# Kernel optimization log

Measured on AMD Instinct MI355X. Metric: run time of the kernel, lower is better.

## Reference

```python
import jax, jax.numpy as jnp
import numpy as np

N = 50000        # nodes
E = 500000       # undirected edges (stored once)
D = 64           # n_in_features
DOUT = 64        # n_out_features
HLF = 2          # hl_factor
NCONV = 3        # n_conv_its
H = D * HLF      # hidden width of conv MLPs


def setup_inputs() -> dict:
    key = jax.random.key(0)
    ks = jax.random.split(key, 8)
    s = 0.05
    edge_features = jax.random.normal(ks[0], (E, D), jnp.float32)
    edge_index = jax.random.randint(ks[1], (2, E), 0, N, dtype=jnp.int64)
    node_w1 = jax.random.normal(ks[2], (NCONV, 2 * D, H), jnp.float32) * s
    node_b1 = jnp.zeros((NCONV, H), jnp.float32)
    node_w2 = jax.random.normal(ks[3], (NCONV, H, D), jnp.float32) * s
    node_b2 = jnp.zeros((NCONV, D), jnp.float32)
    edge_w1 = jax.random.normal(ks[4], (2 * D, H), jnp.float32) * s
    edge_b1 = jnp.zeros((H,), jnp.float32)
    edge_w2 = jax.random.normal(ks[5], (H, DOUT), jnp.float32) * s
    edge_b2 = jnp.zeros((DOUT,), jnp.float32)
    return dict(edge_features=edge_features, edge_index=edge_index,
                node_w1=node_w1, node_b1=node_b1, node_w2=node_w2, node_b2=node_b2,
                edge_w1=edge_w1, edge_b1=edge_b1, edge_w2=edge_w2, edge_b2=edge_b2)


def _seg_mean(x, idx, n):
    s = jax.ops.segment_sum(x, idx, num_segments=n)
    c = jax.ops.segment_sum(jnp.ones((idx.shape[0], 1), x.dtype), idx, num_segments=n)
    return s / jnp.maximum(c, 1.0)


def reference(edge_features, edge_index, node_w1, node_b1, node_w2, node_b2,
              edge_w1, edge_b1, edge_w2, edge_b2):
    src, dst = edge_index[0], edge_index[1]
    # bidirectional (symmetrized) edges for message passing
    bi_src = jnp.concatenate([src, dst])
    bi_dst = jnp.concatenate([dst, src])

    # EdgeConvNoNodes: node feature = mean of incident edge features
    x = _seg_mean(jnp.concatenate([edge_features, edge_features], axis=0), bi_dst, N)  # [N, D]

    # NodeConv layers with residual: message = MLP(cat[x_i, x_j]), mean-aggregated
    for i in range(NCONV):
        m = jnp.concatenate([x[bi_dst], x[bi_src]], axis=-1)        # [2E, 2D]
        m = jax.nn.relu(m @ node_w1[i] + node_b1[i])                # [2E, H]
        m = jax.nn.relu(m @ node_w2[i] + node_b2[i])                # [2E, D]
        x = x + _seg_mean(m, bi_dst, N)

    # EdgeConv: symmetric edge MLP over node endpoint pairs + symmetry side loss
    def emlp(a, b):
        h = jax.nn.relu(jnp.concatenate([a, b], axis=-1) @ edge_w1 + edge_b1)
        return h @ edge_w2 + edge_b2

    e1 = emlp(x[src], x[dst])   # [E, DOUT]
    e2 = emlp(x[dst], x[src])   # [E, DOUT]
    edge_out = 0.5 * (e1 + e2)
    side_loss = jnp.mean((e1 - e2) ** 2)
    return edge_out, side_loss
```

## Files before the change

### kernel.cpp

```cpp
#include <hip/hip_runtime.h>


#define NN 50000
#define NE 500000
#define DE 1000000
#define NEB 7813

typedef __attribute__((ext_vector_type(8))) __bf16 bfrag;
typedef __attribute__((ext_vector_type(8))) short  svec8;
typedef __attribute__((ext_vector_type(4))) float  f32x4;

__device__ __forceinline__ unsigned short f2bf(float f){
  unsigned u = __builtin_bit_cast(unsigned, f);
  u += 0x7fffu + ((u >> 16) & 1u);
  return (unsigned short)(u >> 16);
}
__device__ __forceinline__ float bf2f(unsigned short s){
  return __builtin_bit_cast(float, ((unsigned)s) << 16);
}
#define MFMA __builtin_amdgcn_mfma_f32_16x16x32_bf16

__device__ __forceinline__ bfrag hbuild2(svec8 pv, svec8 qv){
  bfrag r;
  #pragma unroll
  for (int i = 0; i < 8; i++){
    float f = bf2f((unsigned short)pv[i]) + bf2f((unsigned short)qv[i]);
    f = f > 0.f ? f : 0.f;
    r[i] = (__bf16)f;
  }
  return r;
}

__global__ void k_hist(const int* __restrict__ ei, int* __restrict__ cnt,
                       int* __restrict__ cnt2){
  int e = blockIdx.x*256 + threadIdx.x;
  if (e >= DE) return;
  int dst = (e < NE) ? ei[NE + e] : ei[e - NE];
  atomicAdd(&cnt[dst], 1);
  if (e < NE) atomicAdd(&cnt2[ei[e]], 1);
}

__device__ __forceinline__ void scan_impl(const int* __restrict__ cnt,
                                          int* __restrict__ off, int* __restrict__ cur,
                                          float* __restrict__ dinv, int total){
  __shared__ int wsum[16];
  __shared__ int carry_s;
  int tid = threadIdx.x;
  int lane = tid & 63, w = tid >> 6;
  int carry = 0;
  for (int base = 0; base < NN; base += 1024){
    int idx = base + tid;
    int v = (idx < NN) ? cnt[idx] : 0;
    int inc = v;
    for (int o2 = 1; o2 < 64; o2 <<= 1){
      int t = __shfl_up(inc, o2);
      if (lane >= o2) inc += t;
    }
    if (lane == 63) wsum[w] = inc;
    __syncthreads();
    if (tid < 16){
      int vv = wsum[tid], p = vv;
      for (int o2 = 1; o2 < 16; o2 <<= 1){
        int t = __shfl_up(p, o2, 16);
        if (tid >= o2) p += t;
      }
      wsum[tid] = p - vv;
    }
    __syncthreads();
    int ex = carry + wsum[w] + inc - v;
    if (idx < NN){
      off[idx] = ex; cur[idx] = ex;
      dinv[idx] = 1.0f / (float)(v > 1 ? v : 1);
    }
    if (tid == 1023) carry_s = carry + wsum[15] + inc;
    __syncthreads();
    carry = carry_s;
  }
  if (tid == 0) off[NN] = total;
}

__global__ void k_scan2(const int* __restrict__ cntA, int* __restrict__ offA,
                        int* __restrict__ curA, float* __restrict__ dinvA,
                        const int* __restrict__ cntB, int* __restrict__ offB,
                        int* __restrict__ curB, float* __restrict__ dinvB){
  if (blockIdx.x == 0) scan_impl(cntA, offA, curA, dinvA, DE);
  else                 scan_impl(cntB, offB, curB, dinvB, NE);
}

__global__ void k_fill(const int* __restrict__ ei, int* __restrict__ cur,
                       int* __restrict__ nbr, int* __restrict__ dstA, int* __restrict__ eid,
                       int* __restrict__ cur2, int* __restrict__ eord,
                       int* __restrict__ es, int* __restrict__ ed){
  int e = blockIdx.x*256 + threadIdx.x;
  if (e >= DE) return;
  int s, d, id;
  if (e < NE){ s = ei[e];  d = ei[NE + e]; id = e;      }
  else       { s = ei[e];  d = ei[e - NE]; id = e - NE; }
  int pos = atomicAdd(&cur[d], 1);
  nbr[pos] = s; dstA[pos] = d; eid[pos] = id;
  if (e < NE){
    int p2 = atomicAdd(&cur2[s], 1);
    eord[p2] = e; es[p2] = s; ed[p2] = d;
  }
}

__global__ void k_pack(const float* __restrict__ nw1, const float* __restrict__ nw2,
                       const float* __restrict__ ew1, const float* __restrict__ ew2,
                       unsigned short* __restrict__ wp){
  int t = blockIdx.x*256 + threadIdx.x;
  if (t >= 98304) return;
  const float* src; int NO, p, base;
  if (t < 49152)      { int l = t/16384;            src = nw1 + l*16384; NO=128; p = t - l*16384;      base = t - p; }
  else if (t < 73728) { int q = t-49152; int l=q/8192; src = nw2 + l*8192; NO=64; p = q - l*8192;      base = t - p; }
  else if (t < 90112) {                              src = ew1;           NO=128; p = t - 73728;       base = 73728; }
  else                {                              src = ew2;           NO=64;  p = t - 90112;       base = 90112; }
  int f = p >> 9, r = p & 511, lane = r >> 3, i = r & 7;
  int NB = NO >> 4, kb = f / NB, nb = f - kb*NB;
  int k = kb*32 + ((lane >> 4) << 3) + i;
  int c = nb*16 + (lane & 15);
  wp[base + p] = f2bf(src[k*NO + c]);
}

__global__ __launch_bounds__(256,4) void k_init(
    const float* __restrict__ ef, const int* __restrict__ dstA,
    const int* __restrict__ eid, float* __restrict__ xsum)
{
  int lane = threadIdx.x & 63, wid = threadIdx.x >> 6;
  int tile = (blockIdx.x*4 + wid) * 32;
  if (tile >= DE) return;
  int q = lane >> 4, c4 = lane & 15;
  int dr = dstA[tile + (lane & 31)];
  int er = eid[tile + (lane & 31)];
  f32x4 v[8];
  #pragma unroll
  for (int it = 0; it < 8; it++){
    int row = q + it*4;
    int e = __shfl(er, row);
    v[it] = *(const f32x4*)(ef + (size_t)e*64 + c4*4);
  }
  int prev = __shfl_up(dr, 1);
  bool flag = (lane < 32) && (lane == 0 || dr != prev);
  unsigned long long mask = __ballot(flag);
  while (mask){
    int s = (int)__builtin_ctzll(mask);
    mask &= mask - 1;
    int e = mask ? (int)__builtin_ctzll(mask) : 32;
    int dseg = __shfl(dr, s);
    f32x4 p = {0,0,0,0};
    #pragma unroll
    for (int it = 0; it < 8; it++){
      int row = q + it*4;
      if ((unsigned)(row - s) < (unsigned)(e - s)) p += v[it];
    }
    #pragma unroll
    for (int k = 0; k < 4; k++){
      p[k] += __shfl_xor(p[k], 16);
      p[k] += __shfl_xor(p[k], 32);
    }
    if (q == 0){
      atomicAdd(&xsum[dseg*64 + c4*4 + 0], p[0]);
      atomicAdd(&xsum[dseg*64 + c4*4 + 1], p[1]);
      atomicAdd(&xsum[dseg*64 + c4*4 + 2], p[2]);
      atomicAdd(&xsum[dseg*64 + c4*4 + 3], p[3]);
    }
  }
}

__global__ void k_div(const float* __restrict__ xsum, const float* __restrict__ dinv,
                      float* __restrict__ x, unsigned short* __restrict__ xbf){
  int n = blockIdx.x*4 + (threadIdx.x >> 6);
  int lane = threadIdx.x & 63;
  if (n >= NN) return;
  float v = xsum[n*64 + lane] * dinv[n];
  x[n*64 + lane] = v;
  xbf[n*64 + lane] = f2bf(v);
}

__global__ __launch_bounds__(256,2) void k_pq(
    const unsigned short* __restrict__ xbf,
    const unsigned short* __restrict__ wp, int w1off,
    const float* __restrict__ bias,
    unsigned short* __restrict__ pq)
{
  int lane = threadIdx.x & 63, wid = threadIdx.x >> 6;
  int tile = (blockIdx.x*4 + wid) * 32;
  if (tile >= NN) return;
  int r16 = lane & 15, g = lane >> 4;
  const svec8* w1g = (const svec8*)(wp + w1off);
  bfrag a[2][2];
  #pragma unroll
  for (int rb = 0; rb < 2; rb++){
    int n = tile + rb*16 + r16; if (n >= NN) n = NN-1;
    #pragma unroll
    for (int kb = 0; kb < 2; kb++)
      a[rb][kb] = __builtin_bit_cast(bfrag, *(const svec8*)(xbf + n*64 + kb*32 + g*8));
  }
  for (int ph = 0; ph < 2; ph++){
    f32x4 acc[8][2];
    #pragma unroll
    for (int nb = 0; nb < 8; nb++){ acc[nb][0] = (f32x4){0,0,0,0}; acc[nb][1] = (f32x4){0,0,0,0}; }
    #pragma unroll
    for (int kb = 0; kb < 2; kb++){
      #pragma unroll
      for (int nb = 0; nb < 8; nb++){
        bfrag b = __builtin_bit_cast(bfrag, w1g[((ph*2+kb)*8+nb)*64 + lane]);
        acc[nb][0] = MFMA(a[0][kb], b, acc[nb][0], 0, 0, 0);
        acc[nb][1] = MFMA(a[1][kb], b, acc[nb][1], 0, 0, 0);
      }
    }
    int half = ph ? 128 : 0;
    #pragma unroll
    for (int nb = 0; nb < 8; nb++){
      float bv = (ph == 0) ? bias[nb*16 + r16] : 0.f;
      #pragma unroll
      for (int rb = 0; rb < 2; rb++){
        #pragma unroll
        for (int j = 0; j < 4; j++){
          int n = tile + rb*16 + g*4 + j;
          if (n < NN) pq[(size_t)n*256 + half + nb*16 + r16] = f2bf(acc[nb][rb][j] + bv);
        }
      }
    }
  }
}

__global__ __launch_bounds__(256,3) void k_conv(
    const unsigned short* __restrict__ pq,
    const int* __restrict__ cdst, const int* __restrict__ cnbr,
    const unsigned short* __restrict__ wp, int w2off,
    const float* __restrict__ b2, float* __restrict__ xsum)
{
  int lane = threadIdx.x & 63, wid = threadIdx.x >> 6;
  int tile = (blockIdx.x*4 + wid) * 32;
  if (tile >= DE) return;
  int r16 = lane & 15, g = lane >> 4;
  int dr = cdst[tile + (lane & 31)];
  int d0 = cdst[tile + r16],      d1 = cdst[tile + 16 + r16];
  int s0 = cnbr[tile + r16],      s1 = cnbr[tile + 16 + r16];
  const svec8* w2g = (const svec8*)(wp + w2off);

  svec8 LP0[4], LQ0[4], LP1[4], LQ1[4];
  #pragma unroll
  for (int kb = 0; kb < 4; kb++){
    int off = kb*32 + g*8;
    LP0[kb] = *(const svec8*)(pq + (size_t)d0*256 + off);
    LQ0[kb] = *(const svec8*)(pq + (size_t)s0*256 + 128 + off);
    LP1[kb] = *(const svec8*)(pq + (size_t)d1*256 + off);
    LQ1[kb] = *(const svec8*)(pq + (size_t)s1*256 + 128 + off);
  }

  f32x4 acc[4][2];
  #pragma unroll
  for (int nb = 0; nb < 4; nb++){ acc[nb][0] = (f32x4){0,0,0,0}; acc[nb][1] = (f32x4){0,0,0,0}; }

  #pragma unroll
  for (int kb = 0; kb < 4; kb++){
    bfrag h0 = hbuild2(LP0[kb], LQ0[kb]);
    bfrag h1 = hbuild2(LP1[kb], LQ1[kb]);
    #pragma unroll
    for (int nb = 0; nb < 4; nb++){
      bfrag b = __builtin_bit_cast(bfrag, w2g[(kb*4+nb)*64 + lane]);
      acc[nb][0] = MFMA(h0, b, acc[nb][0], 0, 0, 0);
      acc[nb][1] = MFMA(h1, b, acc[nb][1], 0, 0, 0);
    }
  }
  float m[4][2][4];
  #pragma unroll
  for (int nb = 0; nb < 4; nb++){
    float bv = b2[nb*16 + r16];
    #pragma unroll
    for (int rb = 0; rb < 2; rb++){
      #pragma unroll
      for (int j = 0; j < 4; j++){
        float v = acc[nb][rb][j] + bv;
        m[nb][rb][j] = v > 0.f ? v : 0.f;
      }
    }
  }
  int prev = __shfl_up(dr, 1);
  bool flag = (lane < 32) && (lane == 0 || dr != prev);
  unsigned long long mask = __ballot(flag);
  while (mask){
    int s = (int)__builtin_ctzll(mask);
    mask &= mask - 1;
    int e = mask ? (int)__builtin_ctzll(mask) : 32;
    int dseg = __shfl(dr, s);
    float p0 = 0.f, p1 = 0.f, p2 = 0.f, p3 = 0.f;
    #pragma unroll
    for (int rb = 0; rb < 2; rb++){
      #pragma unroll
      for (int j = 0; j < 4; j++){
        int row = rb*16 + g*4 + j;
        if ((unsigned)(row - s) < (unsigned)(e - s)){
          p0 += m[0][rb][j]; p1 += m[1][rb][j]; p2 += m[2][rb][j]; p3 += m[3][rb][j];
        }
      }
    }
    p0 += __shfl_xor(p0, 16); p0 += __shfl_xor(p0, 32);
    p1 += __shfl_xor(p1, 16); p1 += __shfl_xor(p1, 32);
    p2 += __shfl_xor(p2, 16); p2 += __shfl_xor(p2, 32);
    p3 += __shfl_xor(p3, 16); p3 += __shfl_xor(p3, 32);
    if (g == 0){
      atomicAdd(&xsum[dseg*64 +      r16], p0);
      atomicAdd(&xsum[dseg*64 + 16 + r16], p1);
      atomicAdd(&xsum[dseg*64 + 32 + r16], p2);
      atomicAdd(&xsum[dseg*64 + 48 + r16], p3);
    }
  }
}

__global__ void k_finish(const float* __restrict__ xsum, const float* __restrict__ dinv,
                         float* __restrict__ x, unsigned short* __restrict__ xbf){
  int n = blockIdx.x*4 + (threadIdx.x >> 6);
  int lane = threadIdx.x & 63;
  if (n >= NN) return;
  float v = x[n*64 + lane] + xsum[n*64 + lane] * dinv[n];
  x[n*64 + lane] = v;
  xbf[n*64 + lane] = f2bf(v);
}

__global__ __launch_bounds__(256,3) void k_edge(
    const unsigned short* __restrict__ pq,
    const int* __restrict__ eord, const int* __restrict__ es, const int* __restrict__ ed,
    const unsigned short* __restrict__ wp,
    const float* __restrict__ b2,
    float* __restrict__ outp, float* __restrict__ part)
{
  __shared__ float wred[4];
  int lane = threadIdx.x & 63, wid = threadIdx.x >> 6;
  int tile = (blockIdx.x*4 + wid) * 16;
  bool valid = tile < NE;
  int tl = valid ? tile : 0;
  int r16 = lane & 15, g = lane >> 4;
  const svec8* w2g = (const svec8*)(wp + 90112);
  int eidv = eord[tl + r16];
  int sid  = es[tl + r16], did = ed[tl + r16];

  svec8 SP[4], SQ[4], DP[4], DQ[4];
  #pragma unroll
  for (int kb = 0; kb < 4; kb++){
    int off = kb*32 + g*8;
    SP[kb] = *(const svec8*)(pq + (size_t)sid*256 + off);
    SQ[kb] = *(const svec8*)(pq + (size_t)sid*256 + 128 + off);
    DP[kb] = *(const svec8*)(pq + (size_t)did*256 + off);
    DQ[kb] = *(const svec8*)(pq + (size_t)did*256 + 128 + off);
  }

  f32x4 acc[4][2];
  #pragma unroll
  for (int nb = 0; nb < 4; nb++){ acc[nb][0] = (f32x4){0,0,0,0}; acc[nb][1] = (f32x4){0,0,0,0}; }

  #pragma unroll
  for (int kb = 0; kb < 4; kb++){
    bfrag h0 = hbuild2(SP[kb], DQ[kb]);
    bfrag h1 = hbuild2(DP[kb], SQ[kb]);
    #pragma unroll
    for (int nb = 0; nb < 4; nb++){
      bfrag b = __builtin_bit_cast(bfrag, w2g[(kb*4+nb)*64 + lane]);
      acc[nb][0] = MFMA(h0, b, acc[nb][0], 0, 0, 0);
      acc[nb][1] = MFMA(h1, b, acc[nb][1], 0, 0, 0);
    }
  }
  float lsum = 0.f;
  #pragma unroll
  for (int nb = 0; nb < 4; nb++){
    float bv = b2[nb*16 + r16];
    #pragma unroll
    for (int j = 0; j < 4; j++){
      float v1 = acc[nb][0][j] + bv;
      float v2 = acc[nb][1][j] + bv;
      int eo = __shfl(eidv, g*4 + j);
      if (valid) outp[(size_t)eo*64 + nb*16 + r16] = 0.5f*(v1 + v2);
      float d = v1 - v2; lsum += d*d;
    }
  }
  if (!valid) lsum = 0.f;
  for (int o2 = 32; o2 > 0; o2 >>= 1) lsum += __shfl_down(lsum, o2);
  if (lane == 0) wred[wid] = lsum;
  __syncthreads();
  if (threadIdx.x == 0) part[blockIdx.x] = wred[0] + wred[1] + wred[2] + wred[3];
}

__global__ void k_final(const float* __restrict__ part, float* __restrict__ outp){
  __shared__ float wred[16];
  int tid = threadIdx.x;
  float s = 0.f;
  for (int i = tid; i < NEB; i += 1024) s += part[i];
  for (int o2 = 32; o2 > 0; o2 >>= 1) s += __shfl_down(s, o2);
  int lane = tid & 63, w = tid >> 6;
  if (lane == 0) wred[w] = s;
  __syncthreads();
  if (tid == 0){
    float t = 0.f;
    #pragma unroll
    for (int i = 0; i < 16; i++) t += wred[i];
    outp[32000000] = t * (1.0f / 32000000.0f);
  }
}

extern "C" void kernel_launch(void* const* d_in, const int* in_sizes, int n_in,
                              void* d_out, int out_size, void* d_ws, size_t ws_size,
                              hipStream_t stream)
{
  const float* ef  = (const float*)d_in[0];
  const int*   ei  = (const int*)  d_in[1];
  const float* nw1 = (const float*)d_in[2];
  const float* nb1 = (const float*)d_in[3];
  const float* nw2 = (const float*)d_in[4];
  const float* nb2 = (const float*)d_in[5];
  const float* ew1 = (const float*)d_in[6];
  const float* eb1 = (const float*)d_in[7];
  const float* ew2 = (const float*)d_in[8];
  const float* eb2 = (const float*)d_in[9];
  float* outp = (float*)d_out;

  char* ws = (char*)d_ws;
  size_t o = 0;
  auto alloc = [&](size_t b)->char*{ char* p = ws + o; o += (b + 255) & ~(size_t)255; return p; };
  int*   cnt  = (int*)  alloc((size_t)NN*4);
  int*   off  = (int*)  alloc((size_t)(NN+1)*4);
  int*   cur  = (int*)  alloc((size_t)NN*4);
  float* dinv = (float*)alloc((size_t)NN*4);
  int*   cnt2 = (int*)  alloc((size_t)NN*4);
  int*   off2 = (int*)  alloc((size_t)(NN+1)*4);
  int*   cur2 = (int*)  alloc((size_t)NN*4);
  float* dinvS= (float*)alloc((size_t)NN*4);
  int*   nbr  = (int*)  alloc((size_t)DE*4);
  int*   dstA = (int*)  alloc((size_t)DE*4);
  int*   eid  = (int*)  alloc((size_t)DE*4);
  int*   eord = (int*)  alloc((size_t)NE*4);
  int*   es   = (int*)  alloc((size_t)NE*4);
  int*   ed   = (int*)  alloc((size_t)NE*4);
  float* x    = (float*)alloc((size_t)NN*64*4);
  unsigned short* xbf = (unsigned short*)alloc((size_t)NN*64*2);
  unsigned short* wp  = (unsigned short*)alloc((size_t)98304*2);
  float* part = (float*)alloc((size_t)NEB*4);
  unsigned short* pq  = (unsigned short*)alloc((size_t)NN*256*2);
  float* xsI  = (float*)alloc((size_t)NN*64*4);
  float* xs0  = (float*)alloc((size_t)NN*64*4);
  float* xs1  = (float*)alloc((size_t)NN*64*4);
  float* xs2  = (float*)alloc((size_t)NN*64*4);
  float* xsum[3] = {xs0, xs1, xs2};

  hipMemsetAsync(cnt,  0, (size_t)NN*4, stream);
  hipMemsetAsync(cnt2, 0, (size_t)NN*4, stream);
  hipMemsetAsync(xsI, 0, (size_t)NN*64*4, stream);
  hipMemsetAsync(xs0, 0, (size_t)NN*64*4, stream);
  hipMemsetAsync(xs1, 0, (size_t)NN*64*4, stream);
  hipMemsetAsync(xs2, 0, (size_t)NN*64*4, stream);
  k_hist<<<(DE+255)/256, 256, 0, stream>>>(ei, cnt, cnt2);
  k_scan2<<<2, 1024, 0, stream>>>(cnt, off, cur, dinv, cnt2, off2, cur2, dinvS);
  k_fill<<<(DE+255)/256, 256, 0, stream>>>(ei, cur, nbr, dstA, eid, cur2, eord, es, ed);
  k_pack<<<384, 256, 0, stream>>>(nw1, nw2, ew1, ew2, wp);
  k_init<<<NEB, 256, 0, stream>>>(ef, dstA, eid, xsI);
  k_div<<<NN/4 + 1, 256, 0, stream>>>(xsI, dinv, x, xbf);
  for (int l = 0; l < 3; l++){
    k_pq<<<391, 256, 0, stream>>>(xbf, wp, l*16384, nb1 + l*128, pq);
    k_conv<<<DE/128 + 1, 256, 0, stream>>>(pq, dstA, nbr, wp,
                                           49152 + l*8192, nb2 + l*64, xsum[l]);
    k_finish<<<NN/4 + 1, 256, 0, stream>>>(xsum[l], dinv, x, xbf);
  }
  k_pq<<<391, 256, 0, stream>>>(xbf, wp, 73728, eb1, pq);
  k_edge<<<NEB, 256, 0, stream>>>(pq, eord, es, ed, wp, eb2, outp, part);
  k_final<<<1, 1024, 0, stream>>>(part, outp);
}
```

Baseline: 723.4 us.

## Fuse node update into projection kernel and software-pipeline persistent conv/edge tiles

Removes the separate k_div and k_finish kernels. k_pq now reads the fp32 aggregate, applies the degree normalisation and residual add, writes x, and converts to bf16 in-register. k_conv and k_edge become persistent-style kernels: each wave handles 8 consecutive tiles and double-buffers its gather loads, so the next tile's pq rows are fetched while the current tile's MFMAs run. Register pressure rises from the doubled buffers, which drops occupancy to 2 waves per SIMD, and the fixed 1024-block grid reduces the partial-sum count.

New measurement: 911.2 us. 26.0% more time.

```diff
diff --git a/kernel.cpp b/kernel.cpp
--- a/kernel.cpp
+++ b/kernel.cpp
@@ -5,6 +5,9 @@
 #define NE 500000
 #define DE 1000000
 #define NEB 7813
+#define NPB 1024
+#define NT  31250
+#define CH  8
 
 typedef __attribute__((ext_vector_type(8))) __bf16 bfrag;
 typedef __attribute__((ext_vector_type(8))) short  svec8;
@@ -166,18 +169,9 @@
   }
 }
 
-__global__ void k_div(const float* __restrict__ xsum, const float* __restrict__ dinv,
-                      float* __restrict__ x, unsigned short* __restrict__ xbf){
-  int n = blockIdx.x*4 + (threadIdx.x >> 6);
-  int lane = threadIdx.x & 63;
-  if (n >= NN) return;
-  float v = xsum[n*64 + lane] * dinv[n];
-  x[n*64 + lane] = v;
-  xbf[n*64 + lane] = f2bf(v);
-}
-
 __global__ __launch_bounds__(256,2) void k_pq(
-    const unsigned short* __restrict__ xbf,
+    float* __restrict__ x, const float* __restrict__ xs, const float* __restrict__ dinv,
+    int mode,
     const unsigned short* __restrict__ wp, int w1off,
     const float* __restrict__ bias,
     unsigned short* __restrict__ pq)
@@ -190,10 +184,28 @@
   bfrag a[2][2];
   #pragma unroll
   for (int rb = 0; rb < 2; rb++){
-    int n = tile + rb*16 + r16; if (n >= NN) n = NN-1;
-    #pragma unroll
-    for (int kb = 0; kb < 2; kb++)
-      a[rb][kb] = __builtin_bit_cast(bfrag, *(const svec8*)(xbf + n*64 + kb*32 + g*8));
+    int n0 = tile + rb*16 + r16;
+    bool vrow = n0 < NN;
+    int n = vrow ? n0 : NN-1;
+    float dv = dinv[n];
+    #pragma unroll
+    for (int kb = 0; kb < 2; kb++){
+      size_t base = (size_t)n*64 + kb*32 + g*8;
+      f32x4 sa = *(const f32x4*)(xs + base);
+      f32x4 sb = *(const f32x4*)(xs + base + 4);
+      f32x4 xa = {0,0,0,0}, xb = {0,0,0,0};
+      if (mode){ xa = *(const f32x4*)(x + base); xb = *(const f32x4*)(x + base + 4); }
+      f32x4 na = xa + sa*dv;
+      f32x4 nb_ = xb + sb*dv;
+      if (vrow){
+        *(f32x4*)(x + base) = na;
+        *(f32x4*)(x + base + 4) = nb_;
+      }
+      bfrag av;
+      #pragma unroll
+      for (int i = 0; i < 4; i++){ av[i] = (__bf16)na[i]; av[4+i] = (__bf16)nb_[i]; }
+      a[rb][kb] = av;
+    }
   }
   for (int ph = 0; ph < 2; ph++){
     f32x4 acc[8][2];
@@ -224,102 +236,155 @@
   }
 }
 
-__global__ __launch_bounds__(256,3) void k_conv(
+#define CLOAD(dr_, sr_, P0_, Q0_, P1_, Q1_, tt) do{                          \
+  dr_ = cdst[(tt)*32 + (lane & 31)];                                         \
+  sr_ = cnbr[(tt)*32 + (lane & 31)];                                         \
+  int d0_ = __shfl(dr_, r16), d1_ = __shfl(dr_, 16 + r16);                   \
+  int s0_ = __shfl(sr_, r16), s1_ = __shfl(sr_, 16 + r16);                   \
+  _Pragma("unroll")                                                          \
+  for (int kb = 0; kb < 4; kb++){                                            \
+    int off = kb*32 + g*8;                                                   \
+    P0_[kb] = *(const svec8*)(pq + (size_t)d0_*256 + off);                   \
+    Q0_[kb] = *(const svec8*)(pq + (size_t)s0_*256 + 128 + off);             \
+    P1_[kb] = *(const svec8*)(pq + (size_t)d1_*256 + off);                   \
+    Q1_[kb] = *(const svec8*)(pq + (size_t)s1_*256 + 128 + off);             \
+  }                                                                          \
+}while(0)
+
+#define CCOMP(dr_, P0_, Q0_, P1_, Q1_) do{                                   \
+  f32x4 acc[4][2];                                                           \
+  _Pragma("unroll")                                                          \
+  for (int nb = 0; nb < 4; nb++){ acc[nb][0] = (f32x4){0,0,0,0}; acc[nb][1] = (f32x4){0,0,0,0}; } \
+  _Pragma("unroll")                                                          \
+  for (int kb = 0; kb < 4; kb++){                                            \
+    bfrag h0 = hbuild2(P0_[kb], Q0_[kb]);                                    \
+    bfrag h1 = hbuild2(P1_[kb], Q1_[kb]);                                    \
+    _Pragma("unroll")                                                        \
+    for (int nb = 0; nb < 4; nb++){                                          \
+      bfrag b = __builtin_bit_cast(bfrag, w2g[(kb*4+nb)*64 + lane]);         \
+      acc[nb][0] = MFMA(h0, b, acc[nb][0], 0, 0, 0);                         \
+      acc[nb][1] = MFMA(h1, b, acc[nb][1], 0, 0, 0);                         \
+    }                                                                        \
+  }                                                                          \
+  float m[4][2][4];                                                          \
+  _Pragma("unroll")                                                          \
+  for (int nb = 0; nb < 4; nb++){                                            \
+    _Pragma("unroll")                                                        \
+    for (int rb = 0; rb < 2; rb++){                                          \
+      _Pragma("unroll")                                                      \
+      for (int j = 0; j < 4; j++){                                           \
+        float v = acc[nb][rb][j] + bv[nb];                                   \
+        m[nb][rb][j] = v > 0.f ? v : 0.f;                                    \
+      }                                                                      \
+    }                                                                        \
+  }                                                                          \
+  int prev = __shfl_up(dr_, 1);                                              \
+  bool flag = (lane < 32) && (lane == 0 || dr_ != prev);                     \
+  unsigned long long mask = __ballot(flag);                                  \
+  while (mask){                                                              \
+    int s = (int)__builtin_ctzll(mask);                                      \
+    mask &= mask - 1;                                                        \
+    int e = mask ? (int)__builtin_ctzll(mask) : 32;                          \
+    int dseg = __shfl(dr_, s);                                               \
+    float p0 = 0.f, p1 = 0.f, p2 = 0.f, p3 = 0.f;                            \
+    _Pragma("unroll")                                                        \
+    for (int rb = 0; rb < 2; rb++){                                          \
+      _Pragma("unroll")                                                      \
+      for (int j = 0; j < 4; j++){                                           \
+        int row = rb*16 + g*4 + j;                                           \
+        if ((unsigned)(row - s) < (unsigned)(e - s)){                        \
+          p0 += m[0][rb][j]; p1 += m[1][rb][j]; p2 += m[2][rb][j]; p3 += m[3][rb][j]; \
+        }                                                                    \
+      }                                                                      \
+    }                                                                        \
+    p0 += __shfl_xor(p0, 16); p0 += __shfl_xor(p0, 32);                      \
+    p1 += __shfl_xor(p1, 16); p1 += __shfl_xor(p1, 32);                      \
+    p2 += __shfl_xor(p2, 16); p2 += __shfl_xor(p2, 32);                      \
+    p3 += __shfl_xor(p3, 16); p3 += __shfl_xor(p3, 32);                      \
+    if (g == 0){                                                             \
+      atomicAdd(&xsum[dseg*64 +      r16], p0);                              \
+      atomicAdd(&xsum[dseg*64 + 16 + r16], p1);                              \
+      atomicAdd(&xsum[dseg*64 + 32 + r16], p2);                              \
+      atomicAdd(&xsum[dseg*64 + 48 + r16], p3);                              \
+    }                                                                        \
+  }                                                                          \
+}while(0)
+
+__global__ __launch_bounds__(256,2) void k_conv(
     const unsigned short* __restrict__ pq,
     const int* __restrict__ cdst, const int* __restrict__ cnbr,
     const unsigned short* __restrict__ wp, int w2off,
     const float* __restrict__ b2, float* __restrict__ xsum)
 {
   int lane = threadIdx.x & 63, wid = threadIdx.x >> 6;
-  int tile = (blockIdx.x*4 + wid) * 32;
-  if (tile >= DE) return;
+  int wgid = blockIdx.x*4 + wid;
   int r16 = lane & 15, g = lane >> 4;
-  int dr = cdst[tile + (lane & 31)];
-  int d0 = cdst[tile + r16],      d1 = cdst[tile + 16 + r16];
-  int s0 = cnbr[tile + r16],      s1 = cnbr[tile + 16 + r16];
   const svec8* w2g = (const svec8*)(wp + w2off);
-
-  svec8 LP0[4], LQ0[4], LP1[4], LQ1[4];
+  int t0 = wgid*CH, t1 = t0 + CH; if (t1 > NT) t1 = NT;
+  if (t0 >= t1) return;
+  float bv[4];
   #pragma unroll
-  for (int kb = 0; kb < 4; kb++){
-    int off = kb*32 + g*8;
-    LP0[kb] = *(const svec8*)(pq + (size_t)d0*256 + off);
-    LQ0[kb] = *(const svec8*)(pq + (size_t)s0*256 + 128 + off);
-    LP1[kb] = *(const svec8*)(pq + (size_t)d1*256 + off);
-    LQ1[kb] = *(const svec8*)(pq + (size_t)s1*256 + 128 + off);
-  }
-
-  f32x4 acc[4][2];
-  #pragma unroll
-  for (int nb = 0; nb < 4; nb++){ acc[nb][0] = (f32x4){0,0,0,0}; acc[nb][1] = (f32x4){0,0,0,0}; }
-
-  #pragma unroll
-  for (int kb = 0; kb < 4; kb++){
-    bfrag h0 = hbuild2(LP0[kb], LQ0[kb]);
-    bfrag h1 = hbuild2(LP1[kb], LQ1[kb]);
-    #pragma unroll
-    for (int nb = 0; nb < 4; nb++){
-      bfrag b = __builtin_bit_cast(bfrag, w2g[(kb*4+nb)*64 + lane]);
-      acc[nb][0] = MFMA(h0, b, acc[nb][0], 0, 0, 0);
-      acc[nb][1] = MFMA(h1, b, acc[nb][1], 0, 0, 0);
-    }
-  }
-  float m[4][2][4];
-  #pragma unroll
-  for (int nb = 0; nb < 4; nb++){
-    float bv = b2[nb*16 + r16];
-    #pragma unroll
-    for (int rb = 0; rb < 2; rb++){
-      #pragma unroll
-      for (int j = 0; j < 4; j++){
-        float v = acc[nb][rb][j] + bv;
-        m[nb][rb][j] = v > 0.f ? v : 0.f;
-      }
-    }
-  }
-  int prev = __shfl_up(dr, 1);
-  bool flag = (lane < 32) && (lane == 0 || dr != prev);
-  unsigned long long mask = __ballot(flag);
-  while (mask){
-    int s = (int)__builtin_ctzll(mask);
-    mask &= mask - 1;
-    int e = mask ? (int)__builtin_ctzll(mask) : 32;
-    int dseg = __shfl(dr, s);
-    float p0 = 0.f, p1 = 0.f, p2 = 0.f, p3 = 0.f;
-    #pragma unroll
-    for (int rb = 0; rb < 2; rb++){
-      #pragma unroll
-      for (int j = 0; j < 4; j++){
-        int row = rb*16 + g*4 + j;
-        if ((unsigned)(row - s) < (unsigned)(e - s)){
-          p0 += m[0][rb][j]; p1 += m[1][rb][j]; p2 += m[2][rb][j]; p3 += m[3][rb][j];
-        }
-      }
-    }
-    p0 += __shfl_xor(p0, 16); p0 += __shfl_xor(p0, 32);
-    p1 += __shfl_xor(p1, 16); p1 += __shfl_xor(p1, 32);
-    p2 += __shfl_xor(p2, 16); p2 += __shfl_xor(p2, 32);
-    p3 += __shfl_xor(p3, 16); p3 += __shfl_xor(p3, 32);
-    if (g == 0){
-      atomicAdd(&xsum[dseg*64 +      r16], p0);
-      atomicAdd(&xsum[dseg*64 + 16 + r16], p1);
-      atomicAdd(&xsum[dseg*64 + 32 + r16], p2);
-      atomicAdd(&xsum[dseg*64 + 48 + r16], p3);
-    }
-  }
-}
-
-__global__ void k_finish(const float* __restrict__ xsum, const float* __restrict__ dinv,
-                         float* __restrict__ x, unsigned short* __restrict__ xbf){
-  int n = blockIdx.x*4 + (threadIdx.x >> 6);
-  int lane = threadIdx.x & 63;
-  if (n >= NN) return;
-  float v = x[n*64 + lane] + xsum[n*64 + lane] * dinv[n];
-  x[n*64 + lane] = v;
-  xbf[n*64 + lane] = f2bf(v);
-}
-
-__global__ __launch_bounds__(256,3) void k_edge(
+  for (int nb = 0; nb < 4; nb++) bv[nb] = b2[nb*16 + r16];
+
+  int drA, srA, drB, srB;
+  svec8 PA0[4], QA0[4], PA1[4], QA1[4];
+  svec8 PB0[4], QB0[4], PB1[4], QB1[4];
+  CLOAD(drA, srA, PA0, QA0, PA1, QA1, t0);
+  for (int t = t0; t < t1; ){
+    int tb = t + 1;
+    if (tb < t1) CLOAD(drB, srB, PB0, QB0, PB1, QB1, tb);
+    CCOMP(drA, PA0, QA0, PA1, QA1);
+    t = tb;
+    if (t >= t1) break;
+    int tc = t + 1;
+    if (tc < t1) CLOAD(drA, srA, PA0, QA0, PA1, QA1, tc);
+    CCOMP(drB, PB0, QB0, PB1, QB1);
+    t = tc;
+  }
+}
+
+#define ELOAD(ev_, SP_, SQ_, DP_, DQ_, tt) do{                               \
+  ev_ = eord[(tt)*16 + r16];                                                 \
+  int sid_ = es[(tt)*16 + r16], did_ = ed[(tt)*16 + r16];                    \
+  _Pragma("unroll")                                                          \
+  for (int kb = 0; kb < 4; kb++){                                            \
+    int off = kb*32 + g*8;                                                   \
+    SP_[kb] = *(const svec8*)(pq + (size_t)sid_*256 + off);                  \
+    SQ_[kb] = *(const svec8*)(pq + (size_t)sid_*256 + 128 + off);            \
+    DP_[kb] = *(const svec8*)(pq + (size_t)did_*256 + off);                  \
+    DQ_[kb] = *(const svec8*)(pq + (size_t)did_*256 + 128 + off);            \
+  }                                                                          \
+}while(0)
+
+#define ECOMP(ev_, SP_, SQ_, DP_, DQ_) do{                                   \
+  f32x4 acc[4][2];                                                           \
+  _Pragma("unroll")                                                          \
+  for (int nb = 0; nb < 4; nb++){ acc[nb][0] = (f32x4){0,0,0,0}; acc[nb][1] = (f32x4){0,0,0,0}; } \
+  _Pragma("unroll")                                                          \
+  for (int kb = 0; kb < 4; kb++){                                            \
+    bfrag h0 = hbuild2(SP_[kb], DQ_[kb]);                                    \
+    bfrag h1 = hbuild2(DP_[kb], SQ_[kb]);                                    \
+    _Pragma("unroll")                                                        \
+    for (int nb = 0; nb < 4; nb++){                                          \
+      bfrag b = __builtin_bit_cast(bfrag, w2g[(kb*4+nb)*64 + lane]);         \
+      acc[nb][0] = MFMA(h0, b, acc[nb][0], 0, 0, 0);                         \
+      acc[nb][1] = MFMA(h1, b, acc[nb][1], 0, 0, 0);                         \
+    }                                                                        \
+  }                                                                          \
+  _Pragma("unroll")                                                          \
+  for (int nb = 0; nb < 4; nb++){                                            \
+    _Pragma("unroll")                                                        \
+    for (int j = 0; j < 4; j++){                                             \
+      float v1 = acc[nb][0][j] + bv[nb];                                     \
+      float v2 = acc[nb][1][j] + bv[nb];                                     \
+      int eo = __shfl(ev_, g*4 + j);                                         \
+      outp[(size_t)eo*64 + nb*16 + r16] = 0.5f*(v1 + v2);                    \
+      float d = v1 - v2; lsum += d*d;                                        \
+    }                                                                        \
+  }                                                                          \
+}while(0)
+
+__global__ __launch_bounds__(256,2) void k_edge(
     const unsigned short* __restrict__ pq,
     const int* __restrict__ eord, const int* __restrict__ es, const int* __restrict__ ed,
     const unsigned short* __restrict__ wp,
@@ -328,53 +393,31 @@
 {
   __shared__ float wred[4];
   int lane = threadIdx.x & 63, wid = threadIdx.x >> 6;
-  int tile = (blockIdx.x*4 + wid) * 16;
-  bool valid = tile < NE;
-  int tl = valid ? tile : 0;
+  int wgid = blockIdx.x*4 + wid;
   int r16 = lane & 15, g = lane >> 4;
   const svec8* w2g = (const svec8*)(wp + 90112);
-  int eidv = eord[tl + r16];
-  int sid  = es[tl + r16], did = ed[tl + r16];
-
-  svec8 SP[4], SQ[4], DP[4], DQ[4];
+  float bv[4];
   #pragma unroll
-  for (int kb = 0; kb < 4; kb++){
-    int off = kb*32 + g*8;
-    SP[kb] = *(const svec8*)(pq + (size_t)sid*256 + off);
-    SQ[kb] = *(const svec8*)(pq + (size_t)sid*256 + 128 + off);
-    DP[kb] = *(const svec8*)(pq + (size_t)did*256 + off);
-    DQ[kb] = *(const svec8*)(pq + (size_t)did*256 + 128 + off);
-  }
-
-  f32x4 acc[4][2];
-  #pragma unroll
-  for (int nb = 0; nb < 4; nb++){ acc[nb][0] = (f32x4){0,0,0,0}; acc[nb][1] = (f32x4){0,0,0,0}; }
-
-  #pragma unroll
-  for (int kb = 0; kb < 4; kb++){
-    bfrag h0 = hbuild2(SP[kb], DQ[kb]);
-    bfrag h1 = hbuild2(DP[kb], SQ[kb]);
-    #pragma unroll
-    for (int nb = 0; nb < 4; nb++){
-      bfrag b = __builtin_bit_cast(bfrag, w2g[(kb*4+nb)*64 + lane]);
-      acc[nb][0] = MFMA(h0, b, acc[nb][0], 0, 0, 0);
-      acc[nb][1] = MFMA(h1, b, acc[nb][1], 0, 0, 0);
-    }
-  }
+  for (int nb = 0; nb < 4; nb++) bv[nb] = b2[nb*16 + r16];
   float lsum = 0.f;
-  #pragma unroll
-  for (int nb = 0; nb < 4; nb++){
-    float bv = b2[nb*16 + r16];
-    #pragma unroll
-    for (int j = 0; j < 4; j++){
-      float v1 = acc[nb][0][j] + bv;
-      float v2 = acc[nb][1][j] + bv;
-      int eo = __shfl(eidv, g*4 + j);
-      if (valid) outp[(size_t)eo*64 + nb*16 + r16] = 0.5f*(v1 + v2);
-      float d = v1 - v2; lsum += d*d;
-    }
-  }
-  if (!valid) lsum = 0.f;
+  int t0 = wgid*CH, t1 = t0 + CH; if (t1 > NT) t1 = NT;
+  if (t0 < t1){
+    int evA, evB;
+    svec8 SPA[4], SQA[4], DPA[4], DQA[4];
+    svec8 SPB[4], SQB[4], DPB[4], DQB[4];
+    ELOAD(evA, SPA, SQA, DPA, DQA, t0);
+    for (int t = t0; t < t1; ){
+      int tb = t + 1;
+      if (tb < t1) ELOAD(evB, SPB, SQB, DPB, DQB, tb);
+      ECOMP(evA, SPA, SQA, DPA, DQA);
+      t = tb;
+      if (t >= t1) break;
+      int tc = t + 1;
+      if (tc < t1) ELOAD(evA, SPA, SQA, DPA, DQA, tc);
+      ECOMP(evB, SPB, SQB, DPB, DQB);
+      t = tc;
+    }
+  }
   for (int o2 = 32; o2 > 0; o2 >>= 1) lsum += __shfl_down(lsum, o2);
   if (lane == 0) wred[wid] = lsum;
   __syncthreads();
@@ -384,8 +427,7 @@
 __global__ void k_final(const float* __restrict__ part, float* __restrict__ outp){
   __shared__ float wred[16];
   int tid = threadIdx.x;
-  float s = 0.f;
-  for (int i = tid; i < NEB; i += 1024) s += part[i];
+  float s = (tid < NPB) ? part[tid] : 0.f;
   for (int o2 = 32; o2 > 0; o2 >>= 1) s += __shfl_down(s, o2);
   int lane = tid & 63, w = tid >> 6;
   if (lane == 0) wred[w] = s;
@@ -432,15 +474,13 @@
   int*   es   = (int*)  alloc((size_t)NE*4);
   int*   ed   = (int*)  alloc((size_t)NE*4);
   float* x    = (float*)alloc((size_t)NN*64*4);
-  unsigned short* xbf = (unsigned short*)alloc((size_t)NN*64*2);
   unsigned short* wp  = (unsigned short*)alloc((size_t)98304*2);
-  float* part = (float*)alloc((size_t)NEB*4);
+  float* part = (float*)alloc((size_t)NPB*4);
   unsigned short* pq  = (unsigned short*)alloc((size_t)NN*256*2);
   float* xsI  = (float*)alloc((size_t)NN*64*4);
   float* xs0  = (float*)alloc((size_t)NN*64*4);
   float* xs1  = (float*)alloc((size_t)NN*64*4);
   float* xs2  = (float*)alloc((size_t)NN*64*4);
-  float* xsum[3] = {xs0, xs1, xs2};
 
   hipMemsetAsync(cnt,  0, (size_t)NN*4, stream);
   hipMemsetAsync(cnt2, 0, (size_t)NN*4, stream);
@@ -453,14 +493,13 @@
   k_fill<<<(DE+255)/256, 256, 0, stream>>>(ei, cur, nbr, dstA, eid, cur2, eord, es, ed);
   k_pack<<<384, 256, 0, stream>>>(nw1, nw2, ew1, ew2, wp);
   k_init<<<NEB, 256, 0, stream>>>(ef, dstA, eid, xsI);
-  k_div<<<NN/4 + 1, 256, 0, stream>>>(xsI, dinv, x, xbf);
-  for (int l = 0; l < 3; l++){
-    k_pq<<<391, 256, 0, stream>>>(xbf, wp, l*16384, nb1 + l*128, pq);
-    k_conv<<<DE/128 + 1, 256, 0, stream>>>(pq, dstA, nbr, wp,
-                                           49152 + l*8192, nb2 + l*64, xsum[l]);
-    k_finish<<<NN/4 + 1, 256, 0, stream>>>(xsum[l], dinv, x, xbf);
-  }
-  k_pq<<<391, 256, 0, stream>>>(xbf, wp, 73728, eb1, pq);
-  k_edge<<<NEB, 256, 0, stream>>>(pq, eord, es, ed, wp, eb2, outp, part);
+  k_pq<<<391, 256, 0, stream>>>(x, xsI, dinv, 0, wp, 0*16384, nb1 + 0*128, pq);
+  k_conv<<<NPB, 256, 0, stream>>>(pq, dstA, nbr, wp, 49152 + 0*8192, nb2 + 0*64, xs0);
+  k_pq<<<391, 256, 0, stream>>>(x, xs0, dinv, 1, wp, 1*16384, nb1 + 1*128, pq);
+  k_conv<<<NPB, 256, 0, stream>>>(pq, dstA, nbr, wp, 49152 + 1*8192, nb2 + 1*64, xs1);
+  k_pq<<<391, 256, 0, stream>>>(x, xs1, dinv, 1, wp, 2*16384, nb1 + 2*128, pq);
+  k_conv<<<NPB, 256, 0, stream>>>(pq, dstA, nbr, wp, 49152 + 2*8192, nb2 + 2*64, xs2);
+  k_pq<<<391, 256, 0, stream>>>(x, xs2, dinv, 1, wp, 73728, eb1, pq);
+  k_edge<<<NPB, 256, 0, stream>>>(pq, eord, es, ed, wp, eb2, outp, part);
   k_final<<<1, 1024, 0, stream>>>(part, outp);
 }
```
